# Kernel tuning notes

Hardware: AMD Instinct MI355X
Metric: run time of the kernel (lower is better)

Reference implementation:

```python
import jax, jax.numpy as jnp
import numpy as np

EPS = 1e-5  # torch LayerNorm default

def _ln(x):
    # LayerNorm over last dim, no affine (elementwise_affine=False)
    m = jnp.mean(x, axis=-1, keepdims=True)
    v = jnp.var(x, axis=-1, keepdims=True)
    return (x - m) / jnp.sqrt(v + EPS)

def _build_orthogonal(phi):
    """Orthogonal matrix of the 'X' RBS circuit on d qubits (unary subspace).
    phi has 2d-3 angles: a descending diagonal of d-1 adjacent Givens rotations
    followed by an ascending diagonal of d-2. Each RBS(theta) acts on coords
    (k, k+1) as [[cos, sin], [-sin, cos]]."""
    d = (phi.shape[0] + 3) // 2
    W = jnp.eye(d, dtype=phi.dtype)
    wires = list(range(d - 1)) + list(range(d - 3, -1, -1))  # 2d-3 gates
    for g, k in enumerate(wires):
        c, s = jnp.cos(phi[g]), jnp.sin(phi[g])
        rk, rk1 = W[k], W[k + 1]
        W = W.at[k].set(c * rk + s * rk1)
        W = W.at[k + 1].set(-s * rk + c * rk1)
    return W

def setup_inputs() -> dict:
    key = jax.random.key(0)
    ks = jax.random.split(key, 8)
    B, N, E, H, dh = 16, 1024, 512, 8, 64
    return {
        "x": jax.random.normal(ks[0], (B, N, E), jnp.float32),
        "Wv": jax.random.normal(ks[1], (H, dh, dh), jnp.float32) / np.sqrt(dh).astype(np.float32),
        "bv": jnp.zeros((H, dh), jnp.float32),
        "phi": jax.random.uniform(ks[2], (H, 2 * dh - 3), jnp.float32, 0.0, 2.0 * np.pi),
        "W1": jax.random.normal(ks[3], (E, E), jnp.float32) / np.sqrt(E).astype(np.float32),
        "b1": jnp.zeros((E,), jnp.float32),
        "W2": jax.random.normal(ks[4], (E, E), jnp.float32) / np.sqrt(E).astype(np.float32),
        "b2": jnp.zeros((E,), jnp.float32),
    }

def reference(x, Wv, bv, phi, W1, b1, W2, b2):
    B, N, E = x.shape
    H = Wv.shape[0]
    dh = E // H
    xn = _ln(x)                                    # norm1
    xh = xn.reshape(B, N, H, dh)                   # per-head slices
    Worth = jax.vmap(_build_orthogonal)(phi)       # [H, dh, dh]
    # per-head value projection (nn.Linear weights stored as [in, out])
    V = jnp.einsum('bnhd,hde->bnhe', xh, Wv) + bv  # [B,N,H,dh]
    # quantum attention scores: loader(x_j) -> W(phi) -> inverse loader(x_i),
    # rescaled by |x_i||x_j|  ==  A_ij = x_i^T W(phi) x_j
    A = jnp.einsum('bnhd,hde,bmhe->bhnm', xh, Worth, xh)
    P = jax.nn.softmax(A / np.float32(np.sqrt(dh)), axis=-1)
    attn = jnp.einsum('bhnm,bmhe->bnhe', P, V)
    head_out = _ln(attn + xh)                      # per-head LN over dh
    res = head_out.reshape(B, N, E) + x            # MHA + residual
    # merger: Linear -> GELU(exact) -> Linear on norm2(res)
    h = jax.nn.gelu(_ln(res) @ W1 + b1, approximate=False) @ W2 + b2
    return h + res
```

## Files before the change

### kernel.cpp

```cpp
#include <hip/hip_runtime.h>
#include <hip/hip_bf16.h>
#include <math.h>

#define B_  16
#define N_  1024
#define E_  512
#define H_  8

typedef __attribute__((ext_vector_type(8)))  __bf16 bf16x8;
typedef __attribute__((ext_vector_type(4)))  float  f32x4;
typedef __attribute__((ext_vector_type(16))) float  f32x16;
typedef __attribute__((ext_vector_type(4)))  unsigned int u32x4;

struct alignas(16) bf8pack { __hip_bfloat16 v[8]; };
struct alignas(8)  bf4pack { __hip_bfloat16 v[4]; };

static __device__ __forceinline__ float bf2f(__hip_bfloat16 x) { return __bfloat162float(x); }
static __device__ __forceinline__ __hip_bfloat16 f2bf(float x) { return __float2bfloat16(x); }

static __device__ __forceinline__ unsigned pkbf(float lo, float hi) {
    unsigned r;
    asm("v_cvt_pk_bf16_f32 %0, %1, %2" : "=v"(r) : "v"(lo), "v"(hi));
    return r;
}
static __device__ __forceinline__ void swap32(unsigned &a, unsigned &b) {
    asm("v_permlane32_swap_b32 %0, %1" : "+v"(a), "+v"(b));
}
static __device__ __forceinline__ void gload16(const __hip_bfloat16* g, __hip_bfloat16* l) {
    __builtin_amdgcn_global_load_lds(
        (const __attribute__((address_space(1))) unsigned*)g,
        (__attribute__((address_space(3))) unsigned*)l, 16, 0, 0);
}
#define MFMA32(a, b, c) __builtin_amdgcn_mfma_f32_32x32x16_bf16((a), (b), (c), 0, 0, 0)
#define MFMA16(a, b, c) __builtin_amdgcn_mfma_f32_16x16x32_bf16((a), (b), (c), 0, 0, 0)

static __device__ __forceinline__ float gelu_f(float v) {
    float z = fabsf(v) * 0.70710678118654752f;
    float t = 1.0f / fmaf(0.3275911f, z, 1.0f);
    float p = t * fmaf(t, fmaf(t, fmaf(t, fmaf(t, 1.061405429f, -1.453152027f),
                                       1.421413741f), -0.284496736f), 0.254829592f);
    float e = __builtin_amdgcn_exp2f(-z * z * 1.4426950408889634f);
    float erf = 1.0f - p * e;
    erf = copysignf(erf, v);
    return 0.5f * v * (1.0f + erf);
}

__global__ __launch_bounds__(256) void k_prep(const float* __restrict__ phi,
                                              const float* __restrict__ Wv,
                                              const float* __restrict__ W1,
                                              const float* __restrict__ W2,
                                              __hip_bfloat16* __restrict__ worth_t,
                                              __hip_bfloat16* __restrict__ wvt,
                                              __hip_bfloat16* __restrict__ w1t,
                                              __hip_bfloat16* __restrict__ w2t,
                                              float* __restrict__ csum1) {
    __shared__ float sh[64 * 65];
    int tid = threadIdx.x;
    if (blockIdx.x < 128) {
        int bid = blockIdx.x;
        const float* src = (bid & 1) ? W2 : W1;
        __hip_bfloat16* dst = (bid & 1) ? w2t : w1t;
        int tile = bid >> 1;
        int i0 = (tile & 7) * 64, o0 = (tile >> 3) * 64;
        float (*ts)[65] = (float(*)[65])sh;
        int r = tid >> 4, c4 = (tid & 15) * 4;
#pragma unroll
        for (int j4 = 0; j4 < 4; ++j4) {
            float4 v = *reinterpret_cast<const float4*>(&src[(size_t)(i0 + r + 16 * j4) * 512 + o0 + c4]);
            ts[r + 16 * j4][c4 + 0] = v.x; ts[r + 16 * j4][c4 + 1] = v.y;
            ts[r + 16 * j4][c4 + 2] = v.z; ts[r + 16 * j4][c4 + 3] = v.w;
        }
        __syncthreads();
        int o = tid >> 3, cg = tid & 7;
#pragma unroll
        for (int half = 0; half < 2; ++half) {
            int oo = o + 32 * half;
            bf8pack p;
#pragma unroll
            for (int j = 0; j < 8; ++j) p.v[j] = f2bf(ts[cg * 8 + j][oo]);
            *reinterpret_cast<bf8pack*>(&dst[(size_t)(o0 + oo) * 512 + i0 + cg * 8]) = p;
        }
    } else if (blockIdx.x < 136) {
        const float SCL = 0.18033688011112042f;
        int h = blockIdx.x - 128;
        int t = tid;
        if (t < 64) {
            for (int i = 0; i < 64; ++i) sh[i * 65 + t] = (i == t) ? 1.0f : 0.0f;
            for (int g = 0; g < 125; ++g) {
                int k = (g < 63) ? g : (124 - g);
                float ph = phi[h * 125 + g];
                float c = cosf(ph), s = sinf(ph);
                float a  = sh[k * 65 + t];
                float b  = sh[(k + 1) * 65 + t];
                sh[k * 65 + t]       =  c * a + s * b;
                sh[(k + 1) * 65 + t] = -s * a + c * b;
            }
            for (int d = 0; d < 64; ++d)
                worth_t[h * 4096 + t * 64 + d] = f2bf(sh[d * 65 + t] * SCL);
            for (int d = 0; d < 64; ++d)
                wvt[h * 4096 + t * 64 + d] = f2bf(Wv[h * 4096 + d * 64 + t]);
        }
    } else {
        int o = (blockIdx.x - 136) * 256 + tid;
        float s = 0.f;
        for (int i = 0; i < 512; ++i) s += W1[(size_t)i * 512 + o];
        csum1[o] = s;
    }
}

__global__ __launch_bounds__(256) void k_ln1(const float* __restrict__ in,
                                             __hip_bfloat16* __restrict__ out,
                                             __hip_bfloat16* __restrict__ outx) {
    int w = threadIdx.x >> 6, l = threadIdx.x & 63;
    size_t row = (size_t)blockIdx.x * 4 + w;
    const float* p = in + row * 512 + l * 8;
    float4 v0 = *reinterpret_cast<const float4*>(p);
    float4 v1 = *reinterpret_cast<const float4*>(p + 4);
    float vv[8] = {v0.x, v0.y, v0.z, v0.w, v1.x, v1.y, v1.z, v1.w};
    bf8pack xo;
#pragma unroll
    for (int j = 0; j < 8; ++j) xo.v[j] = f2bf(vv[j]);
    *reinterpret_cast<bf8pack*>(outx + row * 512 + l * 8) = xo;
    float s = 0.f, sq = 0.f;
#pragma unroll
    for (int j = 0; j < 8; ++j) { s += vv[j]; sq += vv[j] * vv[j]; }
#pragma unroll
    for (int o = 32; o >= 1; o >>= 1) { s += __shfl_xor(s, o); sq += __shfl_xor(sq, o); }
    float mean = s * (1.0f / 512.0f);
    float var  = sq * (1.0f / 512.0f) - mean * mean;
    float rstd = rsqrtf(var + 1e-5f);
    bf8pack ob;
#pragma unroll
    for (int j = 0; j < 8; ++j) ob.v[j] = f2bf((vv[j] - mean) * rstd);
    *reinterpret_cast<bf8pack*>(out + row * 512 + l * 8) = ob;
}

__global__ __launch_bounds__(256) void k_rowstat(const __hip_bfloat16* __restrict__ res,
                                                 float2* __restrict__ rs) {
    int w = threadIdx.x >> 6, l = threadIdx.x & 63;
    size_t row = (size_t)blockIdx.x * 4 + w;
    bf16x8 u = *reinterpret_cast<const bf16x8*>(res + row * 512 + l * 8);
    float s = 0.f, sq = 0.f;
#pragma unroll
    for (int j = 0; j < 8; ++j) { float a = (float)u[j]; s += a; sq = fmaf(a, a, sq); }
#pragma unroll
    for (int o = 32; o >= 1; o >>= 1) { s += __shfl_xor(s, o); sq += __shfl_xor(sq, o); }
    float mean = s * (1.0f / 512.0f);
    float var  = sq * (1.0f / 512.0f) - mean * mean;
    float rstd = rsqrtf(var + 1e-5f);
    if (l == 0) rs[row] = make_float2(rstd, mean * rstd);
}

__global__ __launch_bounds__(256) void k_proj(const __hip_bfloat16* __restrict__ xn,
                                              const __hip_bfloat16* __restrict__ worth_t,
                                              const __hip_bfloat16* __restrict__ wvt,
                                              const float* __restrict__ bv,
                                              __hip_bfloat16* __restrict__ xw,
                                              __hip_bfloat16* __restrict__ vt) {
    int h = blockIdx.y, rt = blockIdx.x;
    int tid = threadIdx.x, w = tid >> 6, l = tid & 63;
    int lr = l & 15, lg = l >> 4;
    int nw = rt * 64 + w * 16;
    int b  = (rt * 64) >> 10;
    int n0 = (rt * 64) & 1023;
    size_t bh = (size_t)b * H_ + h;

    __shared__ __hip_bfloat16 xw_l[64 * 72];
    __shared__ __hip_bfloat16 vt_l[64 * 72];

    const __hip_bfloat16* xp = xn + (size_t)(nw + lr) * 512 + h * 64 + lg * 8;
    bf16x8 xf0 = *reinterpret_cast<const bf16x8*>(xp);
    bf16x8 xf1 = *reinterpret_cast<const bf16x8*>(xp + 32);

    f32x4 accw[4] = {}, accv[4] = {};
#pragma unroll
    for (int g = 0; g < 4; ++g) {
        const __hip_bfloat16* wp = worth_t + h * 4096 + (g * 16 + lr) * 64 + lg * 8;
        accw[g] = MFMA16(*reinterpret_cast<const bf16x8*>(wp), xf0, accw[g]);
        accw[g] = MFMA16(*reinterpret_cast<const bf16x8*>(wp + 32), xf1, accw[g]);
        const __hip_bfloat16* vp = wvt + h * 4096 + (g * 16 + lr) * 64 + lg * 8;
        accv[g] = MFMA16(xf0, *reinterpret_cast<const bf16x8*>(vp), accv[g]);
        accv[g] = MFMA16(xf1, *reinterpret_cast<const bf16x8*>(vp + 32), accv[g]);
    }
#pragma unroll
    for (int g = 0; g < 4; ++g) {
        bf4pack pw;
#pragma unroll
        for (int r = 0; r < 4; ++r) pw.v[r] = f2bf(accw[g][r]);
        *reinterpret_cast<bf4pack*>(&xw_l[(w * 16 + lr) * 72 + g * 16 + lg * 4]) = pw;
        float bb = bv[h * 64 + g * 16 + lr];
        bf4pack pv;
#pragma unroll
        for (int r = 0; r < 4; ++r) pv.v[r] = f2bf(accv[g][r] + bb);
        *reinterpret_cast<bf4pack*>(&vt_l[(g * 16 + lr) * 72 + w * 16 + lg * 4]) = pv;
    }
    __syncthreads();
    {
        int rr = tid >> 2, c0 = (tid & 3) * 16;
        bf8pack p0 = *reinterpret_cast<const bf8pack*>(&xw_l[rr * 72 + c0]);
        bf8pack p1 = *reinterpret_cast<const bf8pack*>(&xw_l[rr * 72 + c0 + 8]);
        __hip_bfloat16* d1 = xw + (bh * N_ + n0 + rr) * 64 + c0;
        *reinterpret_cast<bf8pack*>(d1)     = p0;
        *reinterpret_cast<bf8pack*>(d1 + 8) = p1;
        bf8pack q0 = *reinterpret_cast<const bf8pack*>(&vt_l[rr * 72 + c0]);
        bf8pack q1 = *reinterpret_cast<const bf8pack*>(&vt_l[rr * 72 + c0 + 8]);
        __hip_bfloat16* d2 = vt + (bh * 64 + rr) * N_ + n0 + c0;
        *reinterpret_cast<bf8pack*>(d2)     = q0;
        *reinterpret_cast<bf8pack*>(d2 + 8) = q1;
    }
}

__global__ __launch_bounds__(512, 4) void k_attn(const __hip_bfloat16* __restrict__ xn,
                                                 const __hip_bfloat16* __restrict__ xw,
                                                 const __hip_bfloat16* __restrict__ vt,
                                                 const __hip_bfloat16* __restrict__ xb,
                                                 __hip_bfloat16* __restrict__ res) {
    int h = blockIdx.x, b = blockIdx.z;
    int tid = threadIdx.x;
    int w = tid >> 6, l = tid & 63;
    int lq = l & 31, hi = l >> 5;
    int q0 = blockIdx.y * 256 + w * 32;
    size_t bh = (size_t)b * H_ + h;

    __shared__ __hip_bfloat16 kb[2][128 * 64];
    __shared__ __hip_bfloat16 vb[2][64 * 128];
    __shared__ float lred[8][32];

    int krow = w * 16 + (l >> 3);
    const __hip_bfloat16* ksrc = xn + ((size_t)b * N_ + krow) * 512 + h * 64
                               + (((l & 7) ^ (krow & 7)) << 3);
    int vrow0 = w * 8 + (l >> 4);
    int vrow1 = vrow0 + 4;
    const __hip_bfloat16* vsrc0 = vt + (bh * 64 + vrow0) * N_ + (((l & 15) ^ (vrow0 & 15)) << 3);
    const __hip_bfloat16* vsrc1 = vt + (bh * 64 + vrow1) * N_ + (((l & 15) ^ (vrow1 & 15)) << 3);

#define STAGE(t) do { int bf_ = (t) & 1; \
        gload16(ksrc + (size_t)((t) * 128) * 512,     &kb[bf_][(w * 16) * 64]); \
        gload16(ksrc + (size_t)((t) * 128 + 8) * 512, &kb[bf_][(w * 16 + 8) * 64]); \
        gload16(vsrc0 + (t) * 128, &vb[bf_][(w * 8) * 128]); \
        gload16(vsrc1 + (t) * 128, &vb[bf_][(w * 8 + 4) * 128]); } while (0)
#define TILE_BAR() do { \
        asm volatile("s_waitcnt vmcnt(0)" ::: "memory"); \
        __builtin_amdgcn_s_barrier(); \
        __builtin_amdgcn_sched_barrier(0); } while (0)

    const __hip_bfloat16* qp = xw + (bh * N_ + q0 + lq) * 64 + 8 * hi;
    bf16x8 qf0 = *reinterpret_cast<const bf16x8*>(qp);
    bf16x8 qf1 = *reinterpret_cast<const bf16x8*>(qp + 16);
    bf16x8 qf2 = *reinterpret_cast<const bf16x8*>(qp + 32);
    bf16x8 qf3 = *reinterpret_cast<const bf16x8*>(qp + 48);

    f32x16 o0 = {}, o1 = {};
    float l_run = 0.f;
    int kso = lq & 7;
    int vso = lq & 15;

    auto body = [&](int bf_, int mm) {
        const __hip_bfloat16* kc = &kb[bf_][mm * 64 * 64];
        const __hip_bfloat16* vc = &vb[bf_][0];
        f32x16 s0 = {}, s1 = {};
        __builtin_amdgcn_s_setprio(1);
#pragma unroll
        for (int kd = 0; kd < 4; ++kd) {
            bf16x8 qf = (kd == 0) ? qf0 : (kd == 1) ? qf1 : (kd == 2) ? qf2 : qf3;
            int sl = ((kd * 2 + hi) ^ kso) << 3;
            bf16x8 ka0 = *reinterpret_cast<const bf16x8*>(kc + lq * 64 + sl);
            bf16x8 ka1 = *reinterpret_cast<const bf16x8*>(kc + (lq + 32) * 64 + sl);
            s0 = MFMA32(ka0, qf, s0);
            s1 = MFMA32(ka1, qf, s1);
        }
        __builtin_amdgcn_s_setprio(0);
#pragma unroll
        for (int i = 0; i < 16; ++i) {
            s0[i] = __builtin_amdgcn_exp2f(s0[i]);
            s1[i] = __builtin_amdgcn_exp2f(s1[i]);
        }
        float ls = 0.f;
#pragma unroll
        for (int i = 0; i < 16; ++i) ls += s0[i] + s1[i];
        l_run += ls;
        bf16x8 pa[4];
        {
            unsigned u0 = pkbf(s0[0], s0[1]), u1 = pkbf(s0[2], s0[3]);
            unsigned u2 = pkbf(s0[4], s0[5]), u3 = pkbf(s0[6], s0[7]);
            swap32(u0, u2); swap32(u1, u3);
            u32x4 uu = {u0, u1, u2, u3};
            pa[0] = __builtin_bit_cast(bf16x8, uu);
        }
        {
            unsigned u0 = pkbf(s0[8], s0[9]),   u1 = pkbf(s0[10], s0[11]);
            unsigned u2 = pkbf(s0[12], s0[13]), u3 = pkbf(s0[14], s0[15]);
            swap32(u0, u2); swap32(u1, u3);
            u32x4 uu = {u0, u1, u2, u3};
            pa[1] = __builtin_bit_cast(bf16x8, uu);
        }
        {
            unsigned u0 = pkbf(s1[0], s1[1]), u1 = pkbf(s1[2], s1[3]);
            unsigned u2 = pkbf(s1[4], s1[5]), u3 = pkbf(s1[6], s1[7]);
            swap32(u0, u2); swap32(u1, u3);
            u32x4 uu = {u0, u1, u2, u3};
            pa[2] = __builtin_bit_cast(bf16x8, uu);
        }
        {
            unsigned u0 = pkbf(s1[8], s1[9]),   u1 = pkbf(s1[10], s1[11]);
            unsigned u2 = pkbf(s1[12], s1[13]), u3 = pkbf(s1[14], s1[15]);
            swap32(u0, u2); swap32(u1, u3);
            u32x4 uu = {u0, u1, u2, u3};
            pa[3] = __builtin_bit_cast(bf16x8, uu);
        }
        __builtin_amdgcn_s_setprio(1);
#pragma unroll
        for (int ks = 0; ks < 4; ++ks) {
            int sl = ((mm * 8 + ks * 2 + hi) ^ vso) << 3;
            bf16x8 v0 = *reinterpret_cast<const bf16x8*>(vc + lq * 128 + sl);
            bf16x8 v1 = *reinterpret_cast<const bf16x8*>(vc + (lq + 32) * 128 + sl);
            o0 = MFMA32(pa[ks], v0, o0);
            o1 = MFMA32(pa[ks], v1, o1);
        }
        __builtin_amdgcn_s_setprio(0);
    };

    STAGE(0);
    TILE_BAR();
    for (int t = 0; t < 7; ++t) {
        STAGE(t + 1);
        body(t & 1, 0);
        body(t & 1, 1);
        TILE_BAR();
    }
    body(1, 0);
    body(1, 1);

    float lt = l_run + __shfl_xor(l_run, 32);
    if (hi == 0) lred[w][lq] = 1.0f / lt;
#pragma unroll
    for (int r = 0; r < 16; ++r) {
        int qr = (r & 3) + 8 * (r >> 2) + 4 * hi;
        float li = lred[w][qr];
        size_t base = ((size_t)b * N_ + q0 + qr) * 512 + h * 64;
        float t0 = o0[r] * li + bf2f(xn[base + lq]);
        float t1 = o1[r] * li + bf2f(xn[base + 32 + lq]);
        float s1v = t0 + t1, s2v = t0 * t0 + t1 * t1;
#pragma unroll
        for (int off = 16; off >= 1; off >>= 1) { s1v += __shfl_xor(s1v, off); s2v += __shfl_xor(s2v, off); }
        float mean = s1v * (1.0f / 64.0f);
        float var  = s2v * (1.0f / 64.0f) - mean * mean;
        float rstd = rsqrtf(var + 1e-5f);
        res[base + lq]      = f2bf((t0 - mean) * rstd + bf2f(xb[base + lq]));
        res[base + 32 + lq] = f2bf((t1 - mean) * rstd + bf2f(xb[base + 32 + lq]));
    }
#undef STAGE
#undef TILE_BAR
}

template <int MODE>
__global__ __launch_bounds__(256, 5) void k_gemm(const __hip_bfloat16* __restrict__ A,
                                                 const __hip_bfloat16* __restrict__ Bt,
                                                 const float* __restrict__ bias,
                                                 const __hip_bfloat16* __restrict__ resid,
                                                 const float2* __restrict__ rstat,
                                                 const float* __restrict__ csum,
                                                 __hip_bfloat16* __restrict__ outb,
                                                 float* __restrict__ outf) {
    int m0 = blockIdx.x * 128, nn0 = blockIdx.y * 64;
    int tid = threadIdx.x, w = tid >> 6, l = tid & 63;
    int lr = l & 15, lg = l >> 4;
    __shared__ __hip_bfloat16 bs[2][64 * 128];

    int srow = w * 16 + (l >> 4);
    int sslot = l & 15;

#define GSTAGE(c) do { \
        _Pragma("unroll") \
        for (int i_ = 0; i_ < 4; ++i_) { \
            int row_ = srow + i_ * 4; \
            gload16(Bt + (size_t)(nn0 + row_) * 512 + (c) * 128 + ((sslot ^ (row_ & 15)) << 3), \
                    &bs[(c) & 1][(w * 16 + i_ * 4) * 128]); \
        } } while (0)

    GSTAGE(0);
    asm volatile("s_waitcnt vmcnt(0)" ::: "memory");
    __builtin_amdgcn_s_barrier();
    __builtin_amdgcn_sched_barrier(0);

    f32x4 acc0[4] = {}, acc1[4] = {};
    const __hip_bfloat16* ap0 = A + (size_t)(m0 + w * 32 + lr) * 512 + lg * 8;
    const __hip_bfloat16* ap1 = ap0 + 16 * 512;
#pragma unroll
    for (int c = 0; c < 4; ++c) {
        if (c < 3) GSTAGE(c + 1);
        const __hip_bfloat16* bc = &bs[c & 1][0];
#pragma unroll
        for (int kk = 0; kk < 4; ++kk) {
            bf16x8 a0 = *reinterpret_cast<const bf16x8*>(ap0 + c * 128 + kk * 32);
            bf16x8 a1 = *reinterpret_cast<const bf16x8*>(ap1 + c * 128 + kk * 32);
#pragma unroll
            for (int g = 0; g < 4; ++g) {
                int row = g * 16 + lr;
                bf16x8 bf = *reinterpret_cast<const bf16x8*>(
                    bc + row * 128 + (((kk * 4 + lg) ^ (row & 15)) << 3));
                acc0[g] = MFMA16(a0, bf, acc0[g]);
                acc1[g] = MFMA16(a1, bf, acc1[g]);
            }
        }
        if (c < 3) {
            asm volatile("s_waitcnt vmcnt(0)" ::: "memory");
            __builtin_amdgcn_s_barrier();
            __builtin_amdgcn_sched_barrier(0);
        }
    }
#undef GSTAGE
    float2 rsA[4], rsB[4];
    if (MODE == 0) {
#pragma unroll
        for (int r = 0; r < 4; ++r) {
            rsA[r] = rstat[m0 + w * 32 + lg * 4 + r];
            rsB[r] = rstat[m0 + w * 32 + lg * 4 + r + 16];
        }
    }
#pragma unroll
    for (int g = 0; g < 4; ++g) {
        int col = nn0 + g * 16 + lr;
        float bb = bias[col];
        float cc = (MODE == 0) ? csum[col] : 0.f;
#pragma unroll
        for (int r = 0; r < 4; ++r) {
            int row0 = m0 + w * 32 + lg * 4 + r;
            if (MODE == 0) {
                float v0 = fmaf(acc0[g][r], rsA[r].x, fmaf(-rsA[r].y, cc, bb));
                float v1 = fmaf(acc1[g][r], rsB[r].x, fmaf(-rsB[r].y, cc, bb));
                outb[(size_t)row0 * 512 + col] = f2bf(gelu_f(v0));
                outb[(size_t)(row0 + 16) * 512 + col] = f2bf(gelu_f(v1));
            } else {
                size_t i0 = (size_t)row0 * 512 + col;
                size_t i1 = (size_t)(row0 + 16) * 512 + col;
                outf[i0] = acc0[g][r] + bb + bf2f(resid[i0]);
                outf[i1] = acc1[g][r] + bb + bf2f(resid[i1]);
            }
        }
    }
}

extern "C" void kernel_launch(void* const* d_in, const int* in_sizes, int n_in,
                              void* d_out, int out_size, void* d_ws, size_t ws_size,
                              hipStream_t stream) {
    const float* x   = (const float*)d_in[0];
    const float* Wv  = (const float*)d_in[1];
    const float* bv  = (const float*)d_in[2];
    const float* phi = (const float*)d_in[3];
    const float* W1  = (const float*)d_in[4];
    const float* b1  = (const float*)d_in[5];
    const float* W2  = (const float*)d_in[6];
    const float* b2  = (const float*)d_in[7];
    float* out = (float*)d_out;

    char* ws = (char*)d_ws;
    __hip_bfloat16* worth_t = (__hip_bfloat16*)(ws + 0);
    __hip_bfloat16* wvt     = (__hip_bfloat16*)(ws + 65536);
    __hip_bfloat16* w1t     = (__hip_bfloat16*)(ws + 131072);
    __hip_bfloat16* w2t     = (__hip_bfloat16*)(ws + 655360);
    float*          csum1   = (float*)(ws + 1179648);
    float2*         rstat   = (float2*)(ws + 1181696);
    __hip_bfloat16* xn      = (__hip_bfloat16*)(ws + 1312768);
    __hip_bfloat16* xw      = (__hip_bfloat16*)(ws + 18089984);
    __hip_bfloat16* vt      = (__hip_bfloat16*)(ws + 34867200);
    __hip_bfloat16* res     = (__hip_bfloat16*)(ws + 51644416);
    __hip_bfloat16* y1      = (__hip_bfloat16*)(ws + 68421632);
    __hip_bfloat16* xb      = (__hip_bfloat16*)(ws + 85198848);

    k_prep<<<dim3(138), dim3(256), 0, stream>>>(phi, Wv, W1, W2, worth_t, wvt, w1t, w2t, csum1);
    k_ln1<<<dim3(4096), dim3(256), 0, stream>>>(x, xn, xb);
    k_proj<<<dim3(256, 8), dim3(256), 0, stream>>>(xn, worth_t, wvt, bv, xw, vt);
    k_attn<<<dim3(8, 4, 16), dim3(512), 0, stream>>>(xn, xw, vt, xb, res);
    k_rowstat<<<dim3(4096), dim3(256), 0, stream>>>(res, rstat);
    k_gemm<0><<<dim3(128, 8), dim3(256), 0, stream>>>(res, w1t, b1, nullptr, rstat, csum1, y1, nullptr);
    k_gemm<1><<<dim3(128, 8), dim3(256), 0, stream>>>(y1, w2t, b2, res, nullptr, nullptr, nullptr, out);
}
```

Measured before the change: 178.3 us.

## Fuse row-stat LayerNorm into GEMM and enlarge GEMM tile to 128x128

Removes the separate row-statistics kernel and computes each 128-row block's mean/rstd inside the first GEMM, keeping them in shared memory. The GEMM tile grows from 128x64 with 256 threads to 128x128 with 512 threads (2x4 warp grid, each warp 64x32), which halves the N-direction block count and cuts redundant A reads. Stats are recomputed redundantly by each of the 4 column blocks, and the larger LDS footprint and register use lower occupancy.

```diff
diff --git a/kernel.cpp b/kernel.cpp
--- a/kernel.cpp
+++ b/kernel.cpp
@@ -135,22 +135,6 @@
     *reinterpret_cast<bf8pack*>(out + row * 512 + l * 8) = ob;
 }
 
-__global__ __launch_bounds__(256) void k_rowstat(const __hip_bfloat16* __restrict__ res,
-                                                 float2* __restrict__ rs) {
-    int w = threadIdx.x >> 6, l = threadIdx.x & 63;
-    size_t row = (size_t)blockIdx.x * 4 + w;
-    bf16x8 u = *reinterpret_cast<const bf16x8*>(res + row * 512 + l * 8);
-    float s = 0.f, sq = 0.f;
-#pragma unroll
-    for (int j = 0; j < 8; ++j) { float a = (float)u[j]; s += a; sq = fmaf(a, a, sq); }
-#pragma unroll
-    for (int o = 32; o >= 1; o >>= 1) { s += __shfl_xor(s, o); sq += __shfl_xor(sq, o); }
-    float mean = s * (1.0f / 512.0f);
-    float var  = sq * (1.0f / 512.0f) - mean * mean;
-    float rstd = rsqrtf(var + 1e-5f);
-    if (l == 0) rs[row] = make_float2(rstd, mean * rstd);
-}
-
 __global__ __launch_bounds__(256) void k_proj(const __hip_bfloat16* __restrict__ xn,
                                               const __hip_bfloat16* __restrict__ worth_t,
                                               const __hip_bfloat16* __restrict__ wvt,
@@ -354,53 +338,73 @@
 }
 
 template <int MODE>
-__global__ __launch_bounds__(256, 5) void k_gemm(const __hip_bfloat16* __restrict__ A,
+__global__ __launch_bounds__(512, 2) void k_gemm(const __hip_bfloat16* __restrict__ A,
                                                  const __hip_bfloat16* __restrict__ Bt,
                                                  const float* __restrict__ bias,
                                                  const __hip_bfloat16* __restrict__ resid,
-                                                 const float2* __restrict__ rstat,
                                                  const float* __restrict__ csum,
                                                  __hip_bfloat16* __restrict__ outb,
                                                  float* __restrict__ outf) {
-    int m0 = blockIdx.x * 128, nn0 = blockIdx.y * 64;
+    int m0 = blockIdx.x * 128, nn0 = blockIdx.y * 128;
     int tid = threadIdx.x, w = tid >> 6, l = tid & 63;
     int lr = l & 15, lg = l >> 4;
-    __shared__ __hip_bfloat16 bs[2][64 * 128];
-
-    int srow = w * 16 + (l >> 4);
-    int sslot = l & 15;
+    int wr = w >> 2, wc = w & 3;
+    __shared__ __hip_bfloat16 bs[2][128 * 128];
+    __shared__ float2 rstat_l[128];
 
 #define GSTAGE(c) do { \
         _Pragma("unroll") \
         for (int i_ = 0; i_ < 4; ++i_) { \
-            int row_ = srow + i_ * 4; \
-            gload16(Bt + (size_t)(nn0 + row_) * 512 + (c) * 128 + ((sslot ^ (row_ & 15)) << 3), \
+            int row_ = w * 16 + i_ * 4 + (l >> 4); \
+            gload16(Bt + (size_t)(nn0 + row_) * 512 + (c) * 128 + (((l & 15) ^ (row_ & 15)) << 3), \
                     &bs[(c) & 1][(w * 16 + i_ * 4) * 128]); \
         } } while (0)
 
     GSTAGE(0);
+
+    if constexpr (MODE == 0) {
+#pragma unroll 4
+        for (int i = 0; i < 16; ++i) {
+            int row = w * 16 + i;
+            bf16x8 u = *reinterpret_cast<const bf16x8*>(A + (size_t)(m0 + row) * 512 + l * 8);
+            float s = 0.f, sq = 0.f;
+#pragma unroll
+            for (int j = 0; j < 8; ++j) { float a = (float)u[j]; s += a; sq = fmaf(a, a, sq); }
+#pragma unroll
+            for (int o = 32; o >= 1; o >>= 1) { s += __shfl_xor(s, o); sq += __shfl_xor(sq, o); }
+            if (l == 0) {
+                float mean = s * (1.0f / 512.0f);
+                float var  = sq * (1.0f / 512.0f) - mean * mean;
+                float rstd = rsqrtf(var + 1e-5f);
+                rstat_l[row] = make_float2(rstd, mean * rstd);
+            }
+        }
+    }
+
     asm volatile("s_waitcnt vmcnt(0)" ::: "memory");
     __builtin_amdgcn_s_barrier();
     __builtin_amdgcn_sched_barrier(0);
 
-    f32x4 acc0[4] = {}, acc1[4] = {};
-    const __hip_bfloat16* ap0 = A + (size_t)(m0 + w * 32 + lr) * 512 + lg * 8;
-    const __hip_bfloat16* ap1 = ap0 + 16 * 512;
+    f32x4 acc[4][2] = {};
+    const __hip_bfloat16* ap = A + (size_t)(m0 + wr * 64 + lr) * 512 + lg * 8;
 #pragma unroll
     for (int c = 0; c < 4; ++c) {
         if (c < 3) GSTAGE(c + 1);
         const __hip_bfloat16* bc = &bs[c & 1][0];
 #pragma unroll
         for (int kk = 0; kk < 4; ++kk) {
-            bf16x8 a0 = *reinterpret_cast<const bf16x8*>(ap0 + c * 128 + kk * 32);
-            bf16x8 a1 = *reinterpret_cast<const bf16x8*>(ap1 + c * 128 + kk * 32);
-#pragma unroll
-            for (int g = 0; g < 4; ++g) {
-                int row = g * 16 + lr;
+            bf16x8 a[4];
+#pragma unroll
+            for (int ar = 0; ar < 4; ++ar)
+                a[ar] = *reinterpret_cast<const bf16x8*>(ap + (size_t)ar * 16 * 512 + c * 128 + kk * 32);
+#pragma unroll
+            for (int bg = 0; bg < 2; ++bg) {
+                int row = wc * 32 + bg * 16 + lr;
                 bf16x8 bf = *reinterpret_cast<const bf16x8*>(
                     bc + row * 128 + (((kk * 4 + lg) ^ (row & 15)) << 3));
-                acc0[g] = MFMA16(a0, bf, acc0[g]);
-                acc1[g] = MFMA16(a1, bf, acc1[g]);
+#pragma unroll
+                for (int ar = 0; ar < 4; ++ar)
+                    acc[ar][bg] = MFMA16(a[ar], bf, acc[ar][bg]);
             }
         }
         if (c < 3) {
@@ -410,32 +414,26 @@
         }
     }
 #undef GSTAGE
-    float2 rsA[4], rsB[4];
-    if (MODE == 0) {
-#pragma unroll
-        for (int r = 0; r < 4; ++r) {
-            rsA[r] = rstat[m0 + w * 32 + lg * 4 + r];
-            rsB[r] = rstat[m0 + w * 32 + lg * 4 + r + 16];
-        }
-    }
-#pragma unroll
-    for (int g = 0; g < 4; ++g) {
-        int col = nn0 + g * 16 + lr;
+
+#pragma unroll
+    for (int bg = 0; bg < 2; ++bg) {
+        int col = nn0 + wc * 32 + bg * 16 + lr;
         float bb = bias[col];
         float cc = (MODE == 0) ? csum[col] : 0.f;
 #pragma unroll
-        for (int r = 0; r < 4; ++r) {
-            int row0 = m0 + w * 32 + lg * 4 + r;
-            if (MODE == 0) {
-                float v0 = fmaf(acc0[g][r], rsA[r].x, fmaf(-rsA[r].y, cc, bb));
-                float v1 = fmaf(acc1[g][r], rsB[r].x, fmaf(-rsB[r].y, cc, bb));
-                outb[(size_t)row0 * 512 + col] = f2bf(gelu_f(v0));
-                outb[(size_t)(row0 + 16) * 512 + col] = f2bf(gelu_f(v1));
-            } else {
-                size_t i0 = (size_t)row0 * 512 + col;
-                size_t i1 = (size_t)(row0 + 16) * 512 + col;
-                outf[i0] = acc0[g][r] + bb + bf2f(resid[i0]);
-                outf[i1] = acc1[g][r] + bb + bf2f(resid[i1]);
+        for (int ar = 0; ar < 4; ++ar) {
+#pragma unroll
+            for (int r = 0; r < 4; ++r) {
+                int lrow = wr * 64 + ar * 16 + lg * 4 + r;
+                int row  = m0 + lrow;
+                if (MODE == 0) {
+                    float2 rs = rstat_l[lrow];
+                    float v = fmaf(acc[ar][bg][r], rs.x, fmaf(-rs.y, cc, bb));
+                    outb[(size_t)row * 512 + col] = f2bf(gelu_f(v));
+                } else {
+                    size_t idx = (size_t)row * 512 + col;
+                    outf[idx] = acc[ar][bg][r] + bb + bf2f(resid[idx]);
+                }
             }
         }
     }
@@ -460,7 +458,6 @@
     __hip_bfloat16* w1t     = (__hip_bfloat16*)(ws + 131072);
     __hip_bfloat16* w2t     = (__hip_bfloat16*)(ws + 655360);
     float*          csum1   = (float*)(ws + 1179648);
-    float2*         rstat   = (float2*)(ws + 1181696);
     __hip_bfloat16* xn      = (__hip_bfloat16*)(ws + 1312768);
     __hip_bfloat16* xw      = (__hip_bfloat16*)(ws + 18089984);
     __hip_bfloat16* vt      = (__hip_bfloat16*)(ws + 34867200);
@@ -472,7 +469,6 @@
     k_ln1<<<dim3(4096), dim3(256), 0, stream>>>(x, xn, xb);
     k_proj<<<dim3(256, 8), dim3(256), 0, stream>>>(xn, worth_t, wvt, bv, xw, vt);
     k_attn<<<dim3(8, 4, 16), dim3(512), 0, stream>>>(xn, xw, vt, xb, res);
-    k_rowstat<<<dim3(4096), dim3(256), 0, stream>>>(res, rstat);
-    k_gemm<0><<<dim3(128, 8), dim3(256), 0, stream>>>(res, w1t, b1, nullptr, rstat, csum1, y1, nullptr);
-    k_gemm<1><<<dim3(128, 8), dim3(256), 0, stream>>>(y1, w2t, b2, res, nullptr, nullptr, nullptr, out);
-}
+    k_gemm<0><<<dim3(128, 4), dim3(512), 0, stream>>>(res, w1t, b1, nullptr, csum1, y1, nullptr);
+    k_gemm<1><<<dim3(128, 4), dim3(512), 0, stream>>>(y1, w2t, b2, res, nullptr, nullptr, out);
+}
```

Measured after the change: 204.0 us. +14.4%, slower.

## Fuse norm2 row statistics into first merger GEMM and parallelize W1 column sums

Applied to the files above, without the earlier changes.

Drops the separate row-statistics kernel. The first GEMM now builds each row's mean and variance from the A fragments it already loads for the MFMA, then passes the values across lanes with shuffles in the epilogue. The W1 column-sum blocks in the prep kernel now use float4 loads and a shared-memory reduction over 8 blocks instead of 2, and sincos uses the fast intrinsic. This saves a kernel launch and a full read of res, at the cost of extra ALU work inside the GEMM k-loop and shuffles in the epilogue.

```diff
diff --git a/kernel.cpp b/kernel.cpp
--- a/kernel.cpp
+++ b/kernel.cpp
@@ -89,7 +89,8 @@
             for (int g = 0; g < 125; ++g) {
                 int k = (g < 63) ? g : (124 - g);
                 float ph = phi[h * 125 + g];
-                float c = cosf(ph), s = sinf(ph);
+                float c, s;
+                __sincosf(ph, &s, &c);
                 float a  = sh[k * 65 + t];
                 float b  = sh[(k + 1) * 65 + t];
                 sh[k * 65 + t]       =  c * a + s * b;
@@ -101,10 +102,23 @@
                 wvt[h * 4096 + t * 64 + d] = f2bf(Wv[h * 4096 + d * 64 + t]);
         }
     } else {
-        int o = (blockIdx.x - 136) * 256 + tid;
-        float s = 0.f;
-        for (int i = 0; i < 512; ++i) s += W1[(size_t)i * 512 + o];
-        csum1[o] = s;
+        int c0 = (blockIdx.x - 136) * 64;
+        float (*acc)[68] = (float(*)[68])sh;
+        int cg = (tid & 15) * 4, rg = tid >> 4;
+        float4 s4 = {0.f, 0.f, 0.f, 0.f};
+        for (int rr = 0; rr < 32; ++rr) {
+            float4 v = *reinterpret_cast<const float4*>(&W1[(size_t)(rg * 32 + rr) * 512 + c0 + cg]);
+            s4.x += v.x; s4.y += v.y; s4.z += v.z; s4.w += v.w;
+        }
+        acc[rg][cg + 0] = s4.x; acc[rg][cg + 1] = s4.y;
+        acc[rg][cg + 2] = s4.z; acc[rg][cg + 3] = s4.w;
+        __syncthreads();
+        if (tid < 64) {
+            float s = 0.f;
+#pragma unroll
+            for (int g = 0; g < 16; ++g) s += acc[g][tid];
+            csum1[c0 + tid] = s;
+        }
     }
 }
 
@@ -133,22 +147,6 @@
 #pragma unroll
     for (int j = 0; j < 8; ++j) ob.v[j] = f2bf((vv[j] - mean) * rstd);
     *reinterpret_cast<bf8pack*>(out + row * 512 + l * 8) = ob;
-}
-
-__global__ __launch_bounds__(256) void k_rowstat(const __hip_bfloat16* __restrict__ res,
-                                                 float2* __restrict__ rs) {
-    int w = threadIdx.x >> 6, l = threadIdx.x & 63;
-    size_t row = (size_t)blockIdx.x * 4 + w;
-    bf16x8 u = *reinterpret_cast<const bf16x8*>(res + row * 512 + l * 8);
-    float s = 0.f, sq = 0.f;
-#pragma unroll
-    for (int j = 0; j < 8; ++j) { float a = (float)u[j]; s += a; sq = fmaf(a, a, sq); }
-#pragma unroll
-    for (int o = 32; o >= 1; o >>= 1) { s += __shfl_xor(s, o); sq += __shfl_xor(sq, o); }
-    float mean = s * (1.0f / 512.0f);
-    float var  = sq * (1.0f / 512.0f) - mean * mean;
-    float rstd = rsqrtf(var + 1e-5f);
-    if (l == 0) rs[row] = make_float2(rstd, mean * rstd);
 }
 
 __global__ __launch_bounds__(256) void k_proj(const __hip_bfloat16* __restrict__ xn,
@@ -358,7 +356,6 @@
                                                  const __hip_bfloat16* __restrict__ Bt,
                                                  const float* __restrict__ bias,
                                                  const __hip_bfloat16* __restrict__ resid,
-                                                 const float2* __restrict__ rstat,
                                                  const float* __restrict__ csum,
                                                  __hip_bfloat16* __restrict__ outb,
                                                  float* __restrict__ outf) {
@@ -384,6 +381,7 @@
     __builtin_amdgcn_sched_barrier(0);
 
     f32x4 acc0[4] = {}, acc1[4] = {};
+    float sA = 0.f, sqA = 0.f, sB = 0.f, sqB = 0.f;
     const __hip_bfloat16* ap0 = A + (size_t)(m0 + w * 32 + lr) * 512 + lg * 8;
     const __hip_bfloat16* ap1 = ap0 + 16 * 512;
 #pragma unroll
@@ -394,6 +392,14 @@
         for (int kk = 0; kk < 4; ++kk) {
             bf16x8 a0 = *reinterpret_cast<const bf16x8*>(ap0 + c * 128 + kk * 32);
             bf16x8 a1 = *reinterpret_cast<const bf16x8*>(ap1 + c * 128 + kk * 32);
+            if constexpr (MODE == 0) {
+#pragma unroll
+                for (int j = 0; j < 8; ++j) {
+                    float f0 = (float)a0[j], f1 = (float)a1[j];
+                    sA += f0; sqA = fmaf(f0, f0, sqA);
+                    sB += f1; sqB = fmaf(f1, f1, sqB);
+                }
+            }
 #pragma unroll
             for (int g = 0; g < 4; ++g) {
                 int row = g * 16 + lr;
@@ -410,13 +416,21 @@
         }
     }
 #undef GSTAGE
-    float2 rsA[4], rsB[4];
-    if (MODE == 0) {
-#pragma unroll
-        for (int r = 0; r < 4; ++r) {
-            rsA[r] = rstat[m0 + w * 32 + lg * 4 + r];
-            rsB[r] = rstat[m0 + w * 32 + lg * 4 + r + 16];
-        }
+
+    float rstdA = 0.f, mrA = 0.f, rstdB = 0.f, mrB = 0.f;
+    if constexpr (MODE == 0) {
+        sA += __shfl_xor(sA, 16);  sA += __shfl_xor(sA, 32);
+        sqA += __shfl_xor(sqA, 16); sqA += __shfl_xor(sqA, 32);
+        sB += __shfl_xor(sB, 16);  sB += __shfl_xor(sB, 32);
+        sqB += __shfl_xor(sqB, 16); sqB += __shfl_xor(sqB, 32);
+        float meanA = sA * (1.0f / 512.0f);
+        float varA  = sqA * (1.0f / 512.0f) - meanA * meanA;
+        rstdA = rsqrtf(varA + 1e-5f);
+        mrA   = meanA * rstdA;
+        float meanB = sB * (1.0f / 512.0f);
+        float varB  = sqB * (1.0f / 512.0f) - meanB * meanB;
+        rstdB = rsqrtf(varB + 1e-5f);
+        mrB   = meanB * rstdB;
     }
 #pragma unroll
     for (int g = 0; g < 4; ++g) {
@@ -427,8 +441,10 @@
         for (int r = 0; r < 4; ++r) {
             int row0 = m0 + w * 32 + lg * 4 + r;
             if (MODE == 0) {
-                float v0 = fmaf(acc0[g][r], rsA[r].x, fmaf(-rsA[r].y, cc, bb));
-                float v1 = fmaf(acc1[g][r], rsB[r].x, fmaf(-rsB[r].y, cc, bb));
+                float rs0 = __shfl(rstdA, lg * 4 + r), mr0 = __shfl(mrA, lg * 4 + r);
+                float rs1 = __shfl(rstdB, lg * 4 + r), mr1 = __shfl(mrB, lg * 4 + r);
+                float v0 = fmaf(acc0[g][r], rs0, fmaf(-mr0, cc, bb));
+                float v1 = fmaf(acc1[g][r], rs1, fmaf(-mr1, cc, bb));
                 outb[(size_t)row0 * 512 + col] = f2bf(gelu_f(v0));
                 outb[(size_t)(row0 + 16) * 512 + col] = f2bf(gelu_f(v1));
             } else {
@@ -460,7 +476,6 @@
     __hip_bfloat16* w1t     = (__hip_bfloat16*)(ws + 131072);
     __hip_bfloat16* w2t     = (__hip_bfloat16*)(ws + 655360);
     float*          csum1   = (float*)(ws + 1179648);
-    float2*         rstat   = (float2*)(ws + 1181696);
     __hip_bfloat16* xn      = (__hip_bfloat16*)(ws + 1312768);
     __hip_bfloat16* xw      = (__hip_bfloat16*)(ws + 18089984);
     __hip_bfloat16* vt      = (__hip_bfloat16*)(ws + 34867200);
@@ -468,11 +483,10 @@
     __hip_bfloat16* y1      = (__hip_bfloat16*)(ws + 68421632);
     __hip_bfloat16* xb      = (__hip_bfloat16*)(ws + 85198848);
 
-    k_prep<<<dim3(138), dim3(256), 0, stream>>>(phi, Wv, W1, W2, worth_t, wvt, w1t, w2t, csum1);
+    k_prep<<<dim3(144), dim3(256), 0, stream>>>(phi, Wv, W1, W2, worth_t, wvt, w1t, w2t, csum1);
     k_ln1<<<dim3(4096), dim3(256), 0, stream>>>(x, xn, xb);
     k_proj<<<dim3(256, 8), dim3(256), 0, stream>>>(xn, worth_t, wvt, bv, xw, vt);
     k_attn<<<dim3(8, 4, 16), dim3(512), 0, stream>>>(xn, xw, vt, xb, res);
-    k_rowstat<<<dim3(4096), dim3(256), 0, stream>>>(res, rstat);
-    k_gemm<0><<<dim3(128, 8), dim3(256), 0, stream>>>(res, w1t, b1, nullptr, rstat, csum1, y1, nullptr);
-    k_gemm<1><<<dim3(128, 8), dim3(256), 0, stream>>>(y1, w2t, b2, res, nullptr, nullptr, nullptr, out);
-}
+    k_gemm<0><<<dim3(128, 8), dim3(256), 0, stream>>>(res, w1t, b1, nullptr, csum1, y1, nullptr);
+    k_gemm<1><<<dim3(128, 8), dim3(256), 0, stream>>>(y1, w2t, b2, res, nullptr, nullptr, out);
+}
```

New measurement: 295.9 us. 1.66x slower.
